# Kernel optimization log

Measured on AMD Instinct MI355X. Metric: run time of the kernel, lower is better.

The kernel has to match this reference:

```python
import jax, jax.numpy as jnp
import numpy as np
from jax import lax

HEADS = 8
DIM_HEAD = 64
SCALE = DIM_HEAD ** -0.5

def conv2d(x, w, stride=1, pad=0):
    return lax.conv_general_dilated(
        x, w, window_strides=(stride, stride),
        padding=[(pad, pad), (pad, pad)],
        dimension_numbers=("NCHW", "OIHW", "NCHW"))

def setup_inputs() -> dict:
    key = jax.random.key(0)
    ks = jax.random.split(key, 5)
    b, dim, H, W = 8, 256, 32, 32
    inner = HEADS * DIM_HEAD  # 512
    x = jax.random.normal(ks[0], (b, dim, H, W), jnp.float32)
    Wq = jax.random.normal(ks[1], (inner, dim, 1, 1), jnp.float32) * 0.05
    Wkv = jax.random.normal(ks[2], (2 * inner, dim, 3, 3), jnp.float32) * 0.05
    Wout = jax.random.normal(ks[3], (dim, inner, 1, 1), jnp.float32) * 0.05
    bout = jnp.zeros((dim,), jnp.float32)
    return {"x": x, "Wq": Wq, "Wkv": Wkv, "Wout": Wout, "bout": bout}

def reference(x, Wq, Wkv, Wout, bout):
    b = x.shape[0]
    h, d = HEADS, DIM_HEAD
    q = conv2d(x, Wq, stride=1, pad=0)        # [b, h*d, H, W]
    kv = conv2d(x, Wkv, stride=1, pad=1)      # [b, 2*h*d, H, W]
    k, v = jnp.split(kv, 2, axis=1)
    out_h, out_w = q.shape[-2:]

    def to_bhnd(t):
        # b (h d) x y -> b h (x y) d
        B, _, X, Y = t.shape
        return t.reshape(B, h, d, X * Y).transpose(0, 1, 3, 2)

    q, k, v = map(to_bhnd, (q, k, v))
    dots = jnp.einsum("bhid,bhjd->bhij", q, k) * SCALE
    attn = jax.nn.softmax(dots, axis=-1)
    out = jnp.einsum("bhij,bhjd->bhid", attn, v)  # [b, h, n, d]
    # b h (x y) d -> b (h d) x y
    out = out.transpose(0, 1, 3, 2).reshape(b, h * d, out_h, out_w)
    out = jax.nn.gelu(out, approximate=False)
    out = conv2d(out, Wout, stride=1, pad=0) + bout[None, :, None, None]
    return out
```

## Files before the change

kernel.cpp:

```cpp
#include <hip/hip_runtime.h>
#include <math.h>

#define BATCH 8
#define DIM   256
#define NPIX  1024
#define DHEAD 64
#define INNER 512
#define KVCH  1024
#define PPIX  1156

typedef _Float16 half8 __attribute__((ext_vector_type(8)));
typedef _Float16 half4 __attribute__((ext_vector_type(4)));
typedef float    f32x4 __attribute__((ext_vector_type(4)));
typedef float    f32x16 __attribute__((ext_vector_type(16)));
#define MFMA16(a, b, c) __builtin_amdgcn_mfma_f32_16x16x32_f16(a, b, c, 0, 0, 0)
#define MFMA32(a, b, c) __builtin_amdgcn_mfma_f32_32x32x16_f16(a, b, c, 0, 0, 0)

static __device__ __forceinline__ float gelu_f(float v) {
    return 0.5f * v * (1.0f + erff(v * 0.70710678118654752440f));
}

static __device__ __forceinline__ void gload16(const _Float16* g, _Float16* l) {
    __builtin_amdgcn_global_load_lds(
        (const __attribute__((address_space(1))) unsigned int*)g,
        (__attribute__((address_space(3))) unsigned int*)l, 16, 0, 0);
}

__global__ __launch_bounds__(256) void prep_kernel(
    const float* __restrict__ Wq, const float* __restrict__ Wkv,
    const float* __restrict__ Wout, const float* __restrict__ x,
    _Float16* __restrict__ Aq, _Float16* __restrict__ Akv,
    _Float16* __restrict__ Aout, _Float16* __restrict__ xtp)
{
    const int bid = blockIdx.x, tid = threadIdx.x;
    if (bid < 512) {
        __shared__ float ts[64][65];
        const int pt = (bid & 15) * 64, ic0 = ((bid >> 4) & 3) * 64, b = bid >> 6;
        const float* xb = x + (((size_t)(b * DIM + ic0)) << 10) + pt;
#pragma unroll
        for (int e = tid; e < 4096; e += 256) {
            int i = e >> 6, p = e & 63;
            ts[i][p] = xb[((size_t)i << 10) + p];
        }
        __syncthreads();
#pragma unroll
        for (int e = tid; e < 512; e += 256) {
            int p = e >> 3, ig = e & 7;
            int gp = pt + p, y = gp >> 5, xc = gp & 31;
            half8 v;
#pragma unroll
            for (int u = 0; u < 8; ++u) v[u] = (_Float16)ts[ig * 8 + u][p];
            *(half8*)&xtp[((size_t)b * PPIX + (y + 1) * 34 + xc + 1) * 256 + ic0 + ig * 8] = v;
        }
    } else if (bid < 10752) {
        const int e = (bid - 512) * 256 + tid;
        if (e < 131072) Aq[e] = (_Float16)Wq[e];
        const int e2 = e - 131072;
        if (e2 >= 0 && e2 < 2359296) {
            int oc = e2 / 2304, r = e2 - oc * 2304;
            int s = r >> 8, ic = r & 255;
            Akv[e2] = (_Float16)Wkv[oc * 2304 + ic * 9 + s];
        }
        const int e3 = e - 131072 - 2359296;
        if (e3 >= 0 && e3 < 131072) Aout[e3] = (_Float16)Wout[e3];
    } else {
        const int he = (bid - 10752) * 256 + tid;
        if (he < 270336) {
            int b = he / 33792;
            int r = he - b * 33792;
            int hp = r >> 8, ic = r & 255;
            int row, col;
            if (hp < 34)      { row = 0;  col = hp; }
            else if (hp < 68) { row = 33; col = hp - 34; }
            else { int k2 = hp - 68; row = 1 + (k2 >> 1); col = (k2 & 1) * 33; }
            xtp[((size_t)b * PPIX + row * 34 + col) * 256 + ic] = (_Float16)0.f;
        }
    }
}

__global__ __launch_bounds__(256) void qkv_gemm_kernel(
    const _Float16* __restrict__ Akv, const _Float16* __restrict__ Aq,
    const _Float16* __restrict__ xtp, _Float16* __restrict__ qt,
    _Float16* __restrict__ ktp, _Float16* __restrict__ vb)
{
    __shared__ _Float16 As[128 * 64];
    __shared__ _Float16 Bs[128 * 64];
    const int nt = blockIdx.x, mt = blockIdx.y, b = blockIdx.z;
    const int tid = threadIdx.x;
    const int w = tid >> 6, lane = tid & 63;
    const int l31 = lane & 31, kh = lane >> 5;
    const int m0 = mt * 128, p0 = nt * 128;
    const int wm = (w >> 1) * 64, wn = (w & 1) * 64;

    const int srow = lane >> 3;
    const int scol = ((lane & 7) ^ srow) * 8;

    const _Float16* agp[4];
    const _Float16* bgp[4];
#pragma unroll
    for (int c = 0; c < 4; ++c) {
        int row = (w * 4 + c) * 8 + srow;
        agp[c] = Akv + (size_t)(m0 + row) * 2304 + scol;
        int p = p0 + row, py = p >> 5, px = p & 31;
        bgp[c] = xtp + ((size_t)b * PPIX + (py + 1) * 34 + px + 1) * 256 + scol;
    }

    f32x16 acc[2][2];
#pragma unroll
    for (int mf = 0; mf < 2; ++mf)
#pragma unroll
        for (int nf = 0; nf < 2; ++nf)
#pragma unroll
            for (int r = 0; r < 16; ++r) acc[mf][nf][r] = 0.f;

    for (int kt = 0; kt < 36; ++kt) {
        __syncthreads();
        const int s = kt >> 2;
        const int doff = (s / 3 - 1) * 34 + (s - (s / 3) * 3) - 1;
        const int boff = doff * 256 + (kt & 3) * 64;
#pragma unroll
        for (int c = 0; c < 4; ++c)
            gload16(agp[c] + kt * 64, &As[(w * 4 + c) * 512]);
#pragma unroll
        for (int c = 0; c < 4; ++c)
            gload16(bgp[c] + boff, &Bs[(w * 4 + c) * 512]);
        __syncthreads();
#pragma unroll
        for (int kc = 0; kc < 4; ++kc) {
            const int cx = ((((kc << 1) | kh) ^ (l31 & 7)) << 3);
            half8 af[2], bf[2];
#pragma unroll
            for (int mf = 0; mf < 2; ++mf)
                af[mf] = *(const half8*)&As[(wm + mf * 32 + l31) * 64 + cx];
#pragma unroll
            for (int nf = 0; nf < 2; ++nf)
                bf[nf] = *(const half8*)&Bs[(wn + nf * 32 + l31) * 64 + cx];
#pragma unroll
            for (int mf = 0; mf < 2; ++mf)
#pragma unroll
                for (int nf = 0; nf < 2; ++nf)
                    acc[mf][nf] = MFMA32(af[mf], bf[nf], acc[mf][nf]);
        }
    }

#pragma unroll
    for (int mf = 0; mf < 2; ++mf) {
        const int mbase = m0 + wm + mf * 32;
        if (mbase >= 512) {
#pragma unroll
            for (int nf = 0; nf < 2; ++nf) {
                const int pix = p0 + wn + nf * 32 + l31;
#pragma unroll
                for (int reg = 0; reg < 16; ++reg) {
                    const int mv = mbase - 512 + (reg & 3) + 8 * (reg >> 2) + 4 * kh;
                    vb[(((size_t)(b * 512 + mv)) << 10) + pix] =
                        (_Float16)acc[mf][nf][reg];
                }
            }
        } else {
            const int h = mbase >> 6;
            const int dbase = (mbase & 63) + kh * 4;
#pragma unroll
            for (int nf = 0; nf < 2; ++nf) {
                const int pix = p0 + wn + nf * 32 + l31;
#pragma unroll
                for (int g = 0; g < 4; ++g) {
                    half4 v4;
#pragma unroll
                    for (int r = 0; r < 4; ++r)
                        v4[r] = (_Float16)acc[mf][nf][g * 4 + r];
                    *(half4*)&ktp[((((size_t)(b * 8 + h)) << 10) + pix) * 64 + dbase + g * 8] = v4;
                }
            }
        }
    }

    if (((mt ^ nt) & 1) == 0) {
        const int mq0 = (mt >> 1) * 128;
#pragma unroll
        for (int mf = 0; mf < 2; ++mf)
#pragma unroll
            for (int nf = 0; nf < 2; ++nf)
#pragma unroll
                for (int r = 0; r < 16; ++r) acc[mf][nf][r] = 0.f;

        const _Float16* aqp[4];
#pragma unroll
        for (int c = 0; c < 4; ++c) {
            int row = (w * 4 + c) * 8 + srow;
            aqp[c] = Aq + (size_t)(mq0 + row) * 256 + scol;
        }
        for (int kt = 0; kt < 4; ++kt) {
            __syncthreads();
#pragma unroll
            for (int c = 0; c < 4; ++c)
                gload16(aqp[c] + kt * 64, &As[(w * 4 + c) * 512]);
#pragma unroll
            for (int c = 0; c < 4; ++c)
                gload16(bgp[c] + kt * 64, &Bs[(w * 4 + c) * 512]);
            __syncthreads();
#pragma unroll
            for (int kc = 0; kc < 4; ++kc) {
                const int cx = ((((kc << 1) | kh) ^ (l31 & 7)) << 3);
                half8 af[2], bf[2];
#pragma unroll
                for (int mf = 0; mf < 2; ++mf)
                    af[mf] = *(const half8*)&As[(wm + mf * 32 + l31) * 64 + cx];
#pragma unroll
                for (int nf = 0; nf < 2; ++nf)
                    bf[nf] = *(const half8*)&Bs[(wn + nf * 32 + l31) * 64 + cx];
#pragma unroll
                for (int mf = 0; mf < 2; ++mf)
#pragma unroll
                    for (int nf = 0; nf < 2; ++nf)
                        acc[mf][nf] = MFMA32(af[mf], bf[nf], acc[mf][nf]);
            }
        }
#pragma unroll
        for (int mf = 0; mf < 2; ++mf) {
            const int mbase = mq0 + wm + mf * 32;
            const int h = mbase >> 6;
            const int dbase = (mbase & 63) + kh * 4;
#pragma unroll
            for (int nf = 0; nf < 2; ++nf) {
                const int pix = p0 + wn + nf * 32 + l31;
#pragma unroll
                for (int g = 0; g < 4; ++g) {
                    half4 v4;
#pragma unroll
                    for (int r = 0; r < 4; ++r)
                        v4[r] = (_Float16)(acc[mf][nf][g * 4 + r] * 0.125f);
                    *(half4*)&qt[((((size_t)(b * 8 + h)) << 10) + pix) * 64 + dbase + g * 8] = v4;
                }
            }
        }
    }
}

template<int M, int K, int KROW>
__global__ __launch_bounds__(256) void out_gemm_kernel(
    const _Float16* __restrict__ A, const _Float16* __restrict__ act,
    float* __restrict__ Cout, const float* __restrict__ bias)
{
    __shared__ _Float16 As[128 * 64];
    __shared__ _Float16 Bs[64 * 64];
    const int nt = blockIdx.x, mt = blockIdx.y, b = blockIdx.z;
    const int tid = threadIdx.x;
    const int w = tid >> 6, lane = tid & 63;
    const int quad = lane >> 4, l15 = lane & 15;
    const int m0 = mt * 128, p0 = nt * 64;
    const int wm = w * 32;
    const f32x4 Z4 = {0.f, 0.f, 0.f, 0.f};

    const int srow = lane >> 3;
    const int scol = ((lane & 7) ^ srow) * 8;

    const _Float16* agp[4];
#pragma unroll
    for (int c = 0; c < 4; ++c) {
        int row = (w * 4 + c) * 8 + srow;
        agp[c] = A + (size_t)(m0 + row) * K + scol;
    }
    const _Float16* bgp[2];
#pragma unroll
    for (int c = 0; c < 2; ++c) {
        int row = (w * 2 + c) * 8 + srow;
        bgp[c] = act + (size_t)(b * NPIX + p0 + row) * KROW + scol;
    }

    f32x4 acc[2][4];
#pragma unroll
    for (int mi = 0; mi < 2; ++mi)
#pragma unroll
        for (int ni = 0; ni < 4; ++ni) acc[mi][ni] = Z4;

    for (int kt = 0; kt < K / 64; ++kt) {
        __syncthreads();
#pragma unroll
        for (int c = 0; c < 4; ++c)
            gload16(agp[c] + kt * 64, &As[(w * 4 + c) * 512]);
#pragma unroll
        for (int c = 0; c < 2; ++c)
            gload16(bgp[c] + kt * 64, &Bs[(w * 2 + c) * 512]);
        __syncthreads();
#pragma unroll
        for (int ks = 0; ks < 2; ++ks) {
            half8 av[2], bv[4];
#pragma unroll
            for (int mi = 0; mi < 2; ++mi) {
                const int r = wm + mi * 16 + l15;
                av[mi] = *(const half8*)&As[r * 64 + (((ks * 4 + quad) ^ (l15 & 7)) << 3)];
            }
#pragma unroll
            for (int ni = 0; ni < 4; ++ni) {
                const int r = ni * 16 + l15;
                bv[ni] = *(const half8*)&Bs[r * 64 + (((ks * 4 + quad) ^ (l15 & 7)) << 3)];
            }
#pragma unroll
            for (int mi = 0; mi < 2; ++mi)
#pragma unroll
                for (int ni = 0; ni < 4; ++ni)
                    acc[mi][ni] = MFMA16(av[mi], bv[ni], acc[mi][ni]);
        }
    }

#pragma unroll
    for (int mi = 0; mi < 2; ++mi) {
#pragma unroll
        for (int r = 0; r < 4; ++r) {
            const int m = m0 + wm + mi * 16 + quad * 4 + r;
            const float bv = bias[m];
#pragma unroll
            for (int ni = 0; ni < 4; ++ni) {
                const int pix = p0 + ni * 16 + l15;
                Cout[(((size_t)(b * M + m)) << 10) + pix] = acc[mi][ni][r] + bv;
            }
        }
    }
}

__global__ __launch_bounds__(256) void attn_kernel(
    const _Float16* __restrict__ qt,
    const _Float16* __restrict__ ktp,
    const _Float16* __restrict__ vbb,
    _Float16* __restrict__ gout)
{
    __shared__ _Float16 Ks[128 * 64];
    __shared__ _Float16 Vs[64 * 128];
    __shared__ _Float16 Pb[128 * 128];
    const int qtile = blockIdx.x, bh = blockIdx.y;
    const int b = bh >> 3, h = bh & 7;
    const int p0 = qtile * 128;
    const int tid = threadIdx.x;
    const int w = tid >> 6, lane = tid & 63;
    const int quad = lane >> 4, l15 = lane & 15;
    const f32x4 Z4 = {0.f, 0.f, 0.f, 0.f};

    half8 ones;
#pragma unroll
    for (int u = 0; u < 8; ++u) ones[u] = (_Float16)1.0f;

    half8 qf[2][2];
    {
        const _Float16* qrow =
            qt + ((((size_t)(bh)) << 10) + p0 + w * 32 + l15) * 64;
#pragma unroll
        for (int iff = 0; iff < 2; ++iff)
#pragma unroll
            for (int ks = 0; ks < 2; ++ks)
                qf[iff][ks] = *(const half8*)(qrow + iff * 16 * 64 + ks * 32 + quad * 8);
    }

    const _Float16* kbase = ktp + ((size_t)bh << 16);
    const _Float16* vbase = vbb + (((size_t)(b * 512 + h * 64)) << 10);

    f32x4 oacc[4][2];
#pragma unroll
    for (int mf = 0; mf < 4; ++mf)
#pragma unroll
        for (int iff = 0; iff < 2; ++iff) oacc[mf][iff] = Z4;
    f32x4 racc[2] = {Z4, Z4};

    const int kchunk = (lane & 7) ^ (lane >> 3);
    for (int kt = 0; kt < 8; ++kt) {
        const int pk = kt * 128;
        __syncthreads();
        const _Float16* kg = kbase + (size_t)pk * 64;
#pragma unroll
        for (int i = 0; i < 4; ++i) {
            const int t = i * 4 + w;
            gload16(kg + (t * 8 + (lane >> 3)) * 64 + kchunk * 8, &Ks[t * 512]);
        }
#pragma unroll
        for (int i = 0; i < 4; ++i) {
            const int t = i * 4 + w;
            const int vd = t * 4 + (lane >> 4);
            gload16(vbase + ((size_t)vd << 10) + pk + (((lane & 15) ^ (vd & 15)) << 3),
                    &Vs[t * 512]);
        }
        __syncthreads();

#pragma unroll
        for (int g = 0; g < 2; ++g) {
            f32x4 s[4][2];
#pragma unroll
            for (int jf2 = 0; jf2 < 4; ++jf2) {
                const int jr = (g * 4 + jf2) * 16 + l15;
                const half8 ka0 = *(const half8*)&Ks[jr * 64 + ((quad ^ (l15 & 7)) << 3)];
                const half8 ka1 = *(const half8*)&Ks[jr * 64 + (((4 + quad) ^ (l15 & 7)) << 3)];
#pragma unroll
                for (int iff = 0; iff < 2; ++iff) {
                    s[jf2][iff] = MFMA16(ka0, qf[iff][0], Z4);
                    s[jf2][iff] = MFMA16(ka1, qf[iff][1], s[jf2][iff]);
                }
            }
#pragma unroll
            for (int jf2 = 0; jf2 < 4; ++jf2) {
#pragma unroll
                for (int iff = 0; iff < 2; ++iff) {
                    half4 pv4;
#pragma unroll
                    for (int r = 0; r < 4; ++r)
                        pv4[r] = (_Float16)__expf(s[jf2][iff][r] - 8.0f);
                    const int i = w * 32 + iff * 16 + l15;
                    const int c = ((g * 4 + jf2) << 1) + (quad >> 1);
                    *(half4*)&Pb[i * 128 + ((c ^ l15) << 3) + ((quad & 1) << 2)] = pv4;
                }
            }
        }
#pragma unroll
        for (int kc = 0; kc < 4; ++kc) {
            half8 bv[2];
#pragma unroll
            for (int iff = 0; iff < 2; ++iff) {
                const int i = w * 32 + iff * 16 + l15;
                bv[iff] = *(const half8*)&Pb[i * 128 + (((kc * 4 + quad) ^ l15) << 3)];
                racc[iff] = MFMA16(ones, bv[iff], racc[iff]);
            }
#pragma unroll
            for (int mf = 0; mf < 4; ++mf) {
                const int vr = mf * 16 + l15;
                const half8 va = *(const half8*)&Vs[vr * 128 + (((kc * 4 + quad) ^ l15) << 3)];
#pragma unroll
                for (int iff = 0; iff < 2; ++iff)
                    oacc[mf][iff] = MFMA16(va, bv[iff], oacc[mf][iff]);
            }
        }
    }

    float rinv[2];
#pragma unroll
    for (int iff = 0; iff < 2; ++iff) rinv[iff] = 1.f / racc[iff][0];

    __syncthreads();
    _Float16* scr = Pb;
#pragma unroll
    for (int mf = 0; mf < 4; ++mf) {
#pragma unroll
        for (int iff = 0; iff < 2; ++iff) {
            half4 o4;
#pragma unroll
            for (int r = 0; r < 4; ++r)
                o4[r] = (_Float16)gelu_f(oacc[mf][iff][r] * rinv[iff]);
            const int i = w * 32 + iff * 16 + l15;
            *(half4*)&scr[i * 72 + mf * 16 + quad * 4] = o4;
        }
    }
    __syncthreads();
    _Float16* go = gout + ((size_t)(b * NPIX + p0)) * INNER + h * 64;
#pragma unroll
    for (int it = 0; it < 4; ++it) {
        const int e = tid + it * 256;
        const int p = e >> 3, dg = e & 7;
        *(half8*)(go + (size_t)p * INNER + dg * 8) = *(const half8*)&scr[p * 72 + dg * 8];
    }
}

extern "C" void kernel_launch(void* const* d_in, const int* in_sizes, int n_in,
                              void* d_out, int out_size, void* d_ws, size_t ws_size,
                              hipStream_t stream)
{
    const float* x    = (const float*)d_in[0];
    const float* Wq   = (const float*)d_in[1];
    const float* Wkv  = (const float*)d_in[2];
    const float* Wout = (const float*)d_in[3];
    const float* bout = (const float*)d_in[4];
    float* out = (float*)d_out;

    _Float16* xtp  = (_Float16*)d_ws;
    _Float16* Aq   = xtp  + (size_t)BATCH * PPIX * DIM;
    _Float16* Akv  = Aq   + (size_t)INNER * DIM;
    _Float16* Aout = Akv  + (size_t)KVCH * 2304;
    _Float16* qt   = Aout + (size_t)DIM * INNER;
    _Float16* vb   = qt   + (size_t)BATCH * NPIX * INNER;
    _Float16* ktp  = vb   + (size_t)BATCH * NPIX * INNER;
    _Float16* gout = ktp  + (size_t)BATCH * NPIX * INNER;

    prep_kernel<<<11808, 256, 0, stream>>>(Wq, Wkv, Wout, x, Aq, Akv, Aout, xtp);
    qkv_gemm_kernel<<<dim3(8, 8, BATCH), 256, 0, stream>>>(Akv, Aq, xtp, qt, ktp, vb);
    attn_kernel<<<dim3(8, 64), 256, 0, stream>>>(qt, ktp, vb, gout);
    out_gemm_kernel<DIM, 512, 512>
        <<<dim3(16, 2, BATCH), 256, 0, stream>>>(Aout, gout, out, bout);
}
```

Baseline: 179.0 us.

## Double-buffer LDS tiles in QKV and output GEMM kernels to overlap loads

Both the QKV GEMM and the output projection GEMM now use two shared-memory buffers per operand. The next K-tile is fetched with global_load_lds while MFMAs run on the current tile, and one barrier per iteration replaces two. The Q sub-GEMM's first tile is also prefetched before the KV epilogue stores, so that load overlaps with them. The aim is to hide global-load latency behind compute, at the cost of doubling LDS per block, which may lower occupancy.

```diff
diff --git a/kernel.cpp b/kernel.cpp
--- a/kernel.cpp
+++ b/kernel.cpp
@@ -83,8 +83,8 @@
     const _Float16* __restrict__ xtp, _Float16* __restrict__ qt,
     _Float16* __restrict__ ktp, _Float16* __restrict__ vb)
 {
-    __shared__ _Float16 As[128 * 64];
-    __shared__ _Float16 Bs[128 * 64];
+    __shared__ _Float16 As[2][128 * 64];
+    __shared__ _Float16 Bs[2][128 * 64];
     const int nt = blockIdx.x, mt = blockIdx.y, b = blockIdx.z;
     const int tid = threadIdx.x;
     const int w = tid >> 6, lane = tid & 63;
@@ -113,33 +113,52 @@
 #pragma unroll
             for (int r = 0; r < 16; ++r) acc[mf][nf][r] = 0.f;
 
-    for (int kt = 0; kt < 36; ++kt) {
-        __syncthreads();
+    auto stageKV = [&](int kt, int buf) {
         const int s = kt >> 2;
         const int doff = (s / 3 - 1) * 34 + (s - (s / 3) * 3) - 1;
         const int boff = doff * 256 + (kt & 3) * 64;
 #pragma unroll
-        for (int c = 0; c < 4; ++c)
-            gload16(agp[c] + kt * 64, &As[(w * 4 + c) * 512]);
-#pragma unroll
-        for (int c = 0; c < 4; ++c)
-            gload16(bgp[c] + boff, &Bs[(w * 4 + c) * 512]);
-        __syncthreads();
+        for (int c = 0; c < 4; ++c) {
+            gload16(agp[c] + kt * 64, &As[buf][(w * 4 + c) * 512]);
+            gload16(bgp[c] + boff,    &Bs[buf][(w * 4 + c) * 512]);
+        }
+    };
+    auto compute = [&](int buf) {
 #pragma unroll
         for (int kc = 0; kc < 4; ++kc) {
             const int cx = ((((kc << 1) | kh) ^ (l31 & 7)) << 3);
             half8 af[2], bf[2];
 #pragma unroll
             for (int mf = 0; mf < 2; ++mf)
-                af[mf] = *(const half8*)&As[(wm + mf * 32 + l31) * 64 + cx];
+                af[mf] = *(const half8*)&As[buf][(wm + mf * 32 + l31) * 64 + cx];
 #pragma unroll
             for (int nf = 0; nf < 2; ++nf)
-                bf[nf] = *(const half8*)&Bs[(wn + nf * 32 + l31) * 64 + cx];
+                bf[nf] = *(const half8*)&Bs[buf][(wn + nf * 32 + l31) * 64 + cx];
 #pragma unroll
             for (int mf = 0; mf < 2; ++mf)
 #pragma unroll
                 for (int nf = 0; nf < 2; ++nf)
                     acc[mf][nf] = MFMA32(af[mf], bf[nf], acc[mf][nf]);
+        }
+    };
+
+    stageKV(0, 0);
+    for (int kt = 0; kt < 36; ++kt) {
+        __syncthreads();
+        if (kt + 1 < 36) stageKV(kt + 1, (kt + 1) & 1);
+        compute(kt & 1);
+    }
+
+    const bool doQ = ((mt ^ nt) & 1) == 0;
+    const int mq0 = (mt >> 1) * 128;
+    const _Float16* aqp[4];
+    if (doQ) {
+#pragma unroll
+        for (int c = 0; c < 4; ++c) {
+            int row = (w * 4 + c) * 8 + srow;
+            aqp[c] = Aq + (size_t)(mq0 + row) * 256 + scol;
+            gload16(aqp[c],     &As[0][(w * 4 + c) * 512]);
+            gload16(bgp[c],     &Bs[0][(w * 4 + c) * 512]);
         }
     }
 
@@ -175,8 +194,7 @@
         }
     }
 
-    if (((mt ^ nt) & 1) == 0) {
-        const int mq0 = (mt >> 1) * 128;
+    if (doQ) {
 #pragma unroll
         for (int mf = 0; mf < 2; ++mf)
 #pragma unroll
@@ -184,37 +202,17 @@
 #pragma unroll
                 for (int r = 0; r < 16; ++r) acc[mf][nf][r] = 0.f;
 
-        const _Float16* aqp[4];
-#pragma unroll
-        for (int c = 0; c < 4; ++c) {
-            int row = (w * 4 + c) * 8 + srow;
-            aqp[c] = Aq + (size_t)(mq0 + row) * 256 + scol;
-        }
         for (int kt = 0; kt < 4; ++kt) {
             __syncthreads();
-#pragma unroll
-            for (int c = 0; c < 4; ++c)
-                gload16(aqp[c] + kt * 64, &As[(w * 4 + c) * 512]);
-#pragma unroll
-            for (int c = 0; c < 4; ++c)
-                gload16(bgp[c] + kt * 64, &Bs[(w * 4 + c) * 512]);
-            __syncthreads();
-#pragma unroll
-            for (int kc = 0; kc < 4; ++kc) {
-                const int cx = ((((kc << 1) | kh) ^ (l31 & 7)) << 3);
-                half8 af[2], bf[2];
-#pragma unroll
-                for (int mf = 0; mf < 2; ++mf)
-                    af[mf] = *(const half8*)&As[(wm + mf * 32 + l31) * 64 + cx];
-#pragma unroll
-                for (int nf = 0; nf < 2; ++nf)
-                    bf[nf] = *(const half8*)&Bs[(wn + nf * 32 + l31) * 64 + cx];
-#pragma unroll
-                for (int mf = 0; mf < 2; ++mf)
-#pragma unroll
-                    for (int nf = 0; nf < 2; ++nf)
-                        acc[mf][nf] = MFMA32(af[mf], bf[nf], acc[mf][nf]);
-            }
+            if (kt + 1 < 4) {
+                const int nb = (kt + 1) & 1;
+#pragma unroll
+                for (int c = 0; c < 4; ++c) {
+                    gload16(aqp[c] + (kt + 1) * 64, &As[nb][(w * 4 + c) * 512]);
+                    gload16(bgp[c] + (kt + 1) * 64, &Bs[nb][(w * 4 + c) * 512]);
+                }
+            }
+            compute(kt & 1);
         }
 #pragma unroll
         for (int mf = 0; mf < 2; ++mf) {
@@ -242,8 +240,8 @@
     const _Float16* __restrict__ A, const _Float16* __restrict__ act,
     float* __restrict__ Cout, const float* __restrict__ bias)
 {
-    __shared__ _Float16 As[128 * 64];
-    __shared__ _Float16 Bs[64 * 64];
+    __shared__ _Float16 As[2][128 * 64];
+    __shared__ _Float16 Bs[2][64 * 64];
     const int nt = blockIdx.x, mt = blockIdx.y, b = blockIdx.z;
     const int tid = threadIdx.x;
     const int w = tid >> 6, lane = tid & 63;
@@ -274,27 +272,32 @@
 #pragma unroll
         for (int ni = 0; ni < 4; ++ni) acc[mi][ni] = Z4;
 
+    auto stage = [&](int kt, int buf) {
+#pragma unroll
+        for (int c = 0; c < 4; ++c)
+            gload16(agp[c] + kt * 64, &As[buf][(w * 4 + c) * 512]);
+#pragma unroll
+        for (int c = 0; c < 2; ++c)
+            gload16(bgp[c] + kt * 64, &Bs[buf][(w * 2 + c) * 512]);
+    };
+
+    stage(0, 0);
     for (int kt = 0; kt < K / 64; ++kt) {
         __syncthreads();
-#pragma unroll
-        for (int c = 0; c < 4; ++c)
-            gload16(agp[c] + kt * 64, &As[(w * 4 + c) * 512]);
-#pragma unroll
-        for (int c = 0; c < 2; ++c)
-            gload16(bgp[c] + kt * 64, &Bs[(w * 2 + c) * 512]);
-        __syncthreads();
+        if (kt + 1 < K / 64) stage(kt + 1, (kt + 1) & 1);
+        const int buf = kt & 1;
 #pragma unroll
         for (int ks = 0; ks < 2; ++ks) {
             half8 av[2], bv[4];
 #pragma unroll
             for (int mi = 0; mi < 2; ++mi) {
                 const int r = wm + mi * 16 + l15;
-                av[mi] = *(const half8*)&As[r * 64 + (((ks * 4 + quad) ^ (l15 & 7)) << 3)];
+                av[mi] = *(const half8*)&As[buf][r * 64 + (((ks * 4 + quad) ^ (l15 & 7)) << 3)];
             }
 #pragma unroll
             for (int ni = 0; ni < 4; ++ni) {
                 const int r = ni * 16 + l15;
-                bv[ni] = *(const half8*)&Bs[r * 64 + (((ks * 4 + quad) ^ (l15 & 7)) << 3)];
+                bv[ni] = *(const half8*)&Bs[buf][r * 64 + (((ks * 4 + quad) ^ (l15 & 7)) << 3)];
             }
 #pragma unroll
             for (int mi = 0; mi < 2; ++mi)
```

New measurement: 186.4 us. +4.1%, slower.
